# Performance work log

Measured on AMD Instinct MI355X. Metric: run time of the kernel, lower is better.

## Reference

```python
import jax, jax.numpy as jnp
import numpy as np

NUM_PPR_NODES = 262144
BATCH = 4096
K = NUM_PPR_NODES // BATCH  # ppr neighbors per batch node
F_IN, H, C = 256, 512, 64


def setup_inputs() -> dict:
    key = jax.random.key(0)
    ks = jax.random.split(key, 6)
    X = jax.random.normal(ks[0], (NUM_PPR_NODES, F_IN), dtype=jnp.float32)
    ppr_scores = jax.random.uniform(ks[1], (NUM_PPR_NODES,), dtype=jnp.float32)
    # sorted batch ids; last element == BATCH-1 so dim_size = ppr_idx[-1]+1 = BATCH
    ppr_idx = jnp.repeat(jnp.arange(BATCH, dtype=jnp.int64), K)
    s1 = 1.0 / np.sqrt(F_IN)
    s2 = 1.0 / np.sqrt(H)
    Wa = jax.random.uniform(ks[2], (F_IN, H), jnp.float32, -s1, s1)
    Wb = jax.random.uniform(ks[3], (H, H), jnp.float32, -s2, s2)
    Wc = jax.random.uniform(ks[4], (H, H), jnp.float32, -s2, s2)
    Wd = jax.random.uniform(ks[5], (H, C), jnp.float32, -s2, s2)
    return {"X": X, "ppr_scores": ppr_scores, "ppr_idx": ppr_idx,
            "Wa": Wa, "Wb": Wb, "Wc": Wc, "Wd": Wd}


def reference(X, ppr_scores, ppr_idx, Wa, Wb, Wc, Wd):
    # embedding MLP (dropout inactive at eval): Linear -> ReLU -> Linear, no bias
    emb = jax.nn.relu(X @ Wa) @ Wb                      # [N, H]
    # weighted scatter-sum over ppr neighborhoods
    weighted = emb * ppr_scores[:, None]                # [N, H]
    agg = jax.ops.segment_sum(weighted, ppr_idx, num_segments=BATCH)  # [B, H]
    # logit MLP: Linear -> ReLU -> Linear, no bias
    logits = jax.nn.relu(agg @ Wc) @ Wd                 # [B, C]
    return logits
```

## Files before the change

### kernel.cpp

```cpp
#include <hip/hip_runtime.h>

typedef short bs8 __attribute__((ext_vector_type(8)));
typedef float fx4 __attribute__((ext_vector_type(4)));

__device__ __forceinline__ unsigned short f2bf(float f) {
    unsigned u = __builtin_bit_cast(unsigned, f);
    u += 0x7FFFu + ((u >> 16) & 1u);
    return (unsigned short)(u >> 16);
}

__device__ __forceinline__ bs8 load_cvt8_nt(const float* p) {
    fx4 u = __builtin_nontemporal_load((const fx4*)p);
    fx4 v = __builtin_nontemporal_load((const fx4*)(p + 4));
    bs8 r;
    r[0] = (short)f2bf(u[0]); r[1] = (short)f2bf(u[1]);
    r[2] = (short)f2bf(u[2]); r[3] = (short)f2bf(u[3]);
    r[4] = (short)f2bf(v[0]); r[5] = (short)f2bf(v[1]);
    r[6] = (short)f2bf(v[2]); r[7] = (short)f2bf(v[3]);
    return r;
}

__global__ void pack_b(const float* __restrict__ src, unsigned short* __restrict__ dst,
                       int KN, int N) {
    const int l = threadIdx.x;
    const int lr = l & 15, lg = l >> 4;
    const int bid = blockIdx.x;
    const int cf = bid / KN, kc = bid % KN;
    const int col  = cf * 16 + lr;
    const int krow = kc * 32 + lg * 8;
    const size_t ob = ((size_t)bid * 64 + l) * 8;
    #pragma unroll
    for (int j = 0; j < 8; ++j)
        dst[ob + j] = f2bf(src[(size_t)(krow + j) * N + col]);
}

__global__ __launch_bounds__(256) void warm(const float* __restrict__ p, float* __restrict__ sink) {
    float s = p[blockIdx.x * 256 + threadIdx.x];
    if (s == 1e30f) sink[0] = s;
}

__global__ __launch_bounds__(256) void wbc_gemm(const float* __restrict__ Wb,
                                                const float* __restrict__ Wc,
                                                float* __restrict__ Wbc) {
    __shared__ float As[32][33];
    __shared__ float Bs[32][33];
    const int tx = threadIdx.x & 15, ty = threadIdx.x >> 4;
    const int i0 = blockIdx.y * 32, j0 = blockIdx.x * 32;
    float c00 = 0.f, c01 = 0.f, c10 = 0.f, c11 = 0.f;
    for (int k0 = 0; k0 < 512; k0 += 32) {
        for (int t = threadIdx.x; t < 1024; t += 256) {
            int r = t >> 5, c = t & 31;
            As[r][c] = Wb[(size_t)(i0 + r) * 512 + k0 + c];
            Bs[r][c] = Wc[(size_t)(k0 + r) * 512 + j0 + c];
        }
        __syncthreads();
        #pragma unroll
        for (int k = 0; k < 32; ++k) {
            float a0 = As[ty * 2][k], a1 = As[ty * 2 + 1][k];
            float b0 = Bs[k][tx * 2], b1 = Bs[k][tx * 2 + 1];
            c00 += a0 * b0; c01 += a0 * b1; c10 += a1 * b0; c11 += a1 * b1;
        }
        __syncthreads();
    }
    Wbc[(size_t)(i0 + ty * 2) * 512 + j0 + tx * 2]         = c00;
    Wbc[(size_t)(i0 + ty * 2) * 512 + j0 + tx * 2 + 1]     = c01;
    Wbc[(size_t)(i0 + ty * 2 + 1) * 512 + j0 + tx * 2]     = c10;
    Wbc[(size_t)(i0 + ty * 2 + 1) * 512 + j0 + tx * 2 + 1] = c11;
}

__global__ __launch_bounds__(256, 4) void k1_fused(
    const float* __restrict__ X, const float* __restrict__ scores,
    const bs8* __restrict__ WaP, unsigned short* __restrict__ aggH) {
    __shared__ unsigned short xt[16384];

    const int tid = threadIdx.x;
    const int seg = blockIdx.x;
    const size_t row0 = (size_t)seg * 64;

    #pragma unroll
    for (int it = 0; it < 8; ++it) {
        const int flat = it * 2048 + tid * 8;
        const int r = flat >> 8, c = flat & 255;
        bs8 v = load_cvt8_nt(X + (row0 + r) * 256 + c);
        int byte = r * 512 + c * 2;
        byte ^= (r & 7) << 4;
        *(bs8*)((char*)xt + byte) = v;
    }
    __syncthreads();

    const int w = tid >> 6, l = tid & 63;
    const int lr = l & 15, lg = l >> 4;

    #pragma unroll 1
    for (int ci = 0; ci < 4; ++ci) {
        const int c32 = w * 4 + ci;
        fx4 acc0[4], acc1[4];
        #pragma unroll
        for (int mf = 0; mf < 4; ++mf) {
            acc0[mf] = (fx4){0.f, 0.f, 0.f, 0.f};
            acc1[mf] = (fx4){0.f, 0.f, 0.f, 0.f};
        }

        const bs8* bp = WaP + (size_t)c32 * 16 * 64 + l;
        #pragma unroll 1
        for (int kc = 0; kc < 8; ++kc) {
            bs8 b0 = bp[kc * 64];
            bs8 b1 = bp[(8 + kc) * 64];
            bs8 a[4];
            #pragma unroll
            for (int mf = 0; mf < 4; ++mf) {
                const int row = mf * 16 + lr;
                const int x = row * 512 + kc * 64 + lg * 16;
                a[mf] = *(const bs8*)((const char*)xt + (x ^ ((row & 7) << 4)));
            }
            #pragma unroll
            for (int mf = 0; mf < 4; ++mf) {
                acc0[mf] = __builtin_amdgcn_mfma_f32_16x16x32_bf16(a[mf], b0, acc0[mf], 0, 0, 0);
                acc1[mf] = __builtin_amdgcn_mfma_f32_16x16x32_bf16(a[mf], b1, acc1[mf], 0, 0, 0);
            }
        }

        float sc0[4][4];
        #pragma unroll
        for (int mf = 0; mf < 4; ++mf) {
            fx4 sv = *(const fx4*)(scores + row0 + mf * 16 + lg * 4);
            sc0[mf][0] = sv[0]; sc0[mf][1] = sv[1]; sc0[mf][2] = sv[2]; sc0[mf][3] = sv[3];
        }
        float p0 = 0.f, p1 = 0.f;
        #pragma unroll
        for (int mf = 0; mf < 4; ++mf)
            #pragma unroll
            for (int r = 0; r < 4; ++r) {
                float v0 = acc0[mf][r], v1 = acc1[mf][r];
                v0 = v0 > 0.f ? v0 : 0.f;
                v1 = v1 > 0.f ? v1 : 0.f;
                p0 += v0 * sc0[mf][r];
                p1 += v1 * sc0[mf][r];
            }
        p0 += __shfl_xor(p0, 16, 64);
        p0 += __shfl_xor(p0, 32, 64);
        p1 += __shfl_xor(p1, 16, 64);
        p1 += __shfl_xor(p1, 32, 64);
        if (lg == 0) {
            aggH[(size_t)seg * 512 + c32 * 32 + lr]      = f2bf(p0);
            aggH[(size_t)seg * 512 + c32 * 32 + 16 + lr] = f2bf(p1);
        }
    }
}

__global__ __launch_bounds__(256) void k2_gemm(
    const unsigned short* __restrict__ aggH, const bs8* __restrict__ WbcP,
    unsigned short* __restrict__ T) {
    const int tid = threadIdx.x;
    const int w = tid >> 6, l = tid & 63, lr = l & 15, lg = l >> 4;
    const int gw = blockIdx.x * 4 + w;
    const int rg = gw >> 3, cg = gw & 7;
    const int r0 = rg * 64, c0 = cg * 64;

    fx4 acc[4][4];
    #pragma unroll
    for (int mf = 0; mf < 4; ++mf)
        #pragma unroll
        for (int nf = 0; nf < 4; ++nf)
            acc[mf][nf] = (fx4){0.f, 0.f, 0.f, 0.f};

    #pragma unroll 1
    for (int kc = 0; kc < 16; ++kc) {
        bs8 a[4], b[4];
        #pragma unroll
        for (int mf = 0; mf < 4; ++mf)
            a[mf] = *(const bs8*)(aggH + (size_t)(r0 + mf * 16 + lr) * 512 + kc * 32 + lg * 8);
        #pragma unroll
        for (int nf = 0; nf < 4; ++nf)
            b[nf] = WbcP[((cg * 4 + nf) * 16 + kc) * 64 + l];
        #pragma unroll
        for (int mf = 0; mf < 4; ++mf)
            #pragma unroll
            for (int nf = 0; nf < 4; ++nf)
                acc[mf][nf] = __builtin_amdgcn_mfma_f32_16x16x32_bf16(
                    a[mf], b[nf], acc[mf][nf], 0, 0, 0);
    }
    #pragma unroll
    for (int mf = 0; mf < 4; ++mf)
        #pragma unroll
        for (int nf = 0; nf < 4; ++nf)
            #pragma unroll
            for (int r = 0; r < 4; ++r) {
                float v = fmaxf(acc[mf][nf][r], 0.f);
                T[(size_t)(r0 + mf * 16 + lg * 4 + r) * 512 + c0 + nf * 16 + lr] = f2bf(v);
            }
}

__global__ __launch_bounds__(256) void k3_gemm(
    const unsigned short* __restrict__ T, const bs8* __restrict__ WdP,
    float* __restrict__ out) {
    const int tid = threadIdx.x;
    const int w = tid >> 6, l = tid & 63, lr = l & 15, lg = l >> 4;
    const int gw = blockIdx.x * 4 + w;
    const int r0 = gw * 64;

    fx4 acc[4][4];
    #pragma unroll
    for (int mf = 0; mf < 4; ++mf)
        #pragma unroll
        for (int nf = 0; nf < 4; ++nf)
            acc[mf][nf] = (fx4){0.f, 0.f, 0.f, 0.f};

    #pragma unroll 1
    for (int kc = 0; kc < 16; ++kc) {
        bs8 a[4], b[4];
        #pragma unroll
        for (int mf = 0; mf < 4; ++mf)
            a[mf] = *(const bs8*)(T + (size_t)(r0 + mf * 16 + lr) * 512 + kc * 32 + lg * 8);
        #pragma unroll
        for (int nf = 0; nf < 4; ++nf)
            b[nf] = WdP[(nf * 16 + kc) * 64 + l];
        #pragma unroll
        for (int mf = 0; mf < 4; ++mf)
            #pragma unroll
            for (int nf = 0; nf < 4; ++nf)
                acc[mf][nf] = __builtin_amdgcn_mfma_f32_16x16x32_bf16(
                    a[mf], b[nf], acc[mf][nf], 0, 0, 0);
    }
    #pragma unroll
    for (int mf = 0; mf < 4; ++mf)
        #pragma unroll
        for (int nf = 0; nf < 4; ++nf)
            #pragma unroll
            for (int r = 0; r < 4; ++r)
                out[(size_t)(r0 + mf * 16 + lg * 4 + r) * 64 + nf * 16 + lr] = acc[mf][nf][r];
}

extern "C" void kernel_launch(void* const* d_in, const int* in_sizes, int n_in,
                              void* d_out, int out_size, void* d_ws, size_t ws_size,
                              hipStream_t stream) {
    const float* X  = (const float*)d_in[0];
    const float* sc = (const float*)d_in[1];
    const float* Wa = (const float*)d_in[3];
    const float* Wb = (const float*)d_in[4];
    const float* Wc = (const float*)d_in[5];
    const float* Wd = (const float*)d_in[6];
    float* out = (float*)d_out;

    char* ws = (char*)d_ws;
    unsigned short* WaP  = (unsigned short*)(ws + 0);
    unsigned short* WbcP = (unsigned short*)(ws + 262144);
    unsigned short* WdP  = (unsigned short*)(ws + 786432);
    float*          Wbc  = (float*)         (ws + 851968);
    unsigned short* aggH = (unsigned short*)(ws + 1900544);
    unsigned short* T    = (unsigned short*)(ws + 6094848);
    float*          sink = (float*)         (ws + 11534336);

    pack_b<<<dim3(32 * 8),  dim3(64), 0, stream>>>(Wa,  WaP,  8,  512);
    wbc_gemm<<<dim3(16, 16), dim3(256), 0, stream>>>(Wb, Wc, Wbc);
    pack_b<<<dim3(32 * 16), dim3(64), 0, stream>>>(Wbc, WbcP, 16, 512);
    pack_b<<<dim3(4 * 16),  dim3(64), 0, stream>>>(Wd,  WdP,  16, 64);

    warm<<<dim3(256), dim3(256), 0, stream>>>((const float*)WaP, sink);

    k1_fused<<<dim3(4096), dim3(256), 0, stream>>>(X, sc, (const bs8*)WaP, aggH);
    k2_gemm<<<dim3(128),   dim3(256), 0, stream>>>(aggH, (const bs8*)WbcP, T);
    k3_gemm<<<dim3(16),    dim3(256), 0, stream>>>(T, (const bs8*)WdP, out);
}
```

Measured before the change: 176.0 us.

## Replicate packed Wa across eight copies and preload B fragments in k1

The packed Wa weights are replicated into eight copies in the workspace, and each k1 block reads the copy chosen by blockIdx mod 8, so concurrent blocks spread their weight reads over different addresses and cache channels. The k1 inner loop now loads all sixteen B fragments for a column chunk into registers before the MFMA loop and fully unrolls it, so global loads overlap with compute. Launch bounds drop to three blocks per CU to make room for the extra registers, and the warm kernel grows to touch every replica. The costs are more workspace, extra pack work and lower occupancy.

```diff
diff --git a/kernel.cpp b/kernel.cpp
--- a/kernel.cpp
+++ b/kernel.cpp
@@ -21,7 +21,7 @@
 }
 
 __global__ void pack_b(const float* __restrict__ src, unsigned short* __restrict__ dst,
-                       int KN, int N) {
+                       int KN, int N, int nrep, int rep_stride) {
     const int l = threadIdx.x;
     const int lr = l & 15, lg = l >> 4;
     const int bid = blockIdx.x;
@@ -29,9 +29,14 @@
     const int col  = cf * 16 + lr;
     const int krow = kc * 32 + lg * 8;
     const size_t ob = ((size_t)bid * 64 + l) * 8;
+    unsigned short v[8];
     #pragma unroll
     for (int j = 0; j < 8; ++j)
-        dst[ob + j] = f2bf(src[(size_t)(krow + j) * N + col]);
+        v[j] = f2bf(src[(size_t)(krow + j) * N + col]);
+    for (int rep = 0; rep < nrep; ++rep)
+        #pragma unroll
+        for (int j = 0; j < 8; ++j)
+            dst[(size_t)rep * rep_stride + ob + j] = v[j];
 }
 
 __global__ __launch_bounds__(256) void warm(const float* __restrict__ p, float* __restrict__ sink) {
@@ -68,7 +73,7 @@
     Wbc[(size_t)(i0 + ty * 2 + 1) * 512 + j0 + tx * 2 + 1] = c11;
 }
 
-__global__ __launch_bounds__(256, 4) void k1_fused(
+__global__ __launch_bounds__(256, 3) void k1_fused(
     const float* __restrict__ X, const float* __restrict__ scores,
     const bs8* __restrict__ WaP, unsigned short* __restrict__ aggH) {
     __shared__ unsigned short xt[16384];
@@ -76,6 +81,7 @@
     const int tid = threadIdx.x;
     const int seg = blockIdx.x;
     const size_t row0 = (size_t)seg * 64;
+    const bs8* wp = WaP + (size_t)(blockIdx.x & 7) * 16384;
 
     #pragma unroll
     for (int it = 0; it < 8; ++it) {
@@ -94,6 +100,14 @@
     #pragma unroll 1
     for (int ci = 0; ci < 4; ++ci) {
         const int c32 = w * 4 + ci;
+
+        const bs8* bp = wp + (size_t)c32 * 16 * 64 + l;
+        bs8 b0[8], b1[8];
+        #pragma unroll
+        for (int kc = 0; kc < 8; ++kc) b0[kc] = bp[kc * 64];
+        #pragma unroll
+        for (int kc = 0; kc < 8; ++kc) b1[kc] = bp[(8 + kc) * 64];
+
         fx4 acc0[4], acc1[4];
         #pragma unroll
         for (int mf = 0; mf < 4; ++mf) {
@@ -101,11 +115,8 @@
             acc1[mf] = (fx4){0.f, 0.f, 0.f, 0.f};
         }
 
-        const bs8* bp = WaP + (size_t)c32 * 16 * 64 + l;
-        #pragma unroll 1
+        #pragma unroll
         for (int kc = 0; kc < 8; ++kc) {
-            bs8 b0 = bp[kc * 64];
-            bs8 b1 = bp[(8 + kc) * 64];
             bs8 a[4];
             #pragma unroll
             for (int mf = 0; mf < 4; ++mf) {
@@ -115,8 +126,8 @@
             }
             #pragma unroll
             for (int mf = 0; mf < 4; ++mf) {
-                acc0[mf] = __builtin_amdgcn_mfma_f32_16x16x32_bf16(a[mf], b0, acc0[mf], 0, 0, 0);
-                acc1[mf] = __builtin_amdgcn_mfma_f32_16x16x32_bf16(a[mf], b1, acc1[mf], 0, 0, 0);
+                acc0[mf] = __builtin_amdgcn_mfma_f32_16x16x32_bf16(a[mf], b0[kc], acc0[mf], 0, 0, 0);
+                acc1[mf] = __builtin_amdgcn_mfma_f32_16x16x32_bf16(a[mf], b1[kc], acc1[mf], 0, 0, 0);
             }
         }
 
@@ -244,19 +255,19 @@
 
     char* ws = (char*)d_ws;
     unsigned short* WaP  = (unsigned short*)(ws + 0);
-    unsigned short* WbcP = (unsigned short*)(ws + 262144);
-    unsigned short* WdP  = (unsigned short*)(ws + 786432);
-    float*          Wbc  = (float*)         (ws + 851968);
-    unsigned short* aggH = (unsigned short*)(ws + 1900544);
-    unsigned short* T    = (unsigned short*)(ws + 6094848);
-    float*          sink = (float*)         (ws + 11534336);
-
-    pack_b<<<dim3(32 * 8),  dim3(64), 0, stream>>>(Wa,  WaP,  8,  512);
+    unsigned short* WbcP = (unsigned short*)(ws + 2097152);
+    unsigned short* WdP  = (unsigned short*)(ws + 2621440);
+    float*          Wbc  = (float*)         (ws + 2686976);
+    unsigned short* aggH = (unsigned short*)(ws + 3735552);
+    unsigned short* T    = (unsigned short*)(ws + 7929856);
+    float*          sink = (float*)         (ws + 12124160);
+
+    pack_b<<<dim3(32 * 8),  dim3(64), 0, stream>>>(Wa,  WaP,  8,  512, 8, 131072);
     wbc_gemm<<<dim3(16, 16), dim3(256), 0, stream>>>(Wb, Wc, Wbc);
-    pack_b<<<dim3(32 * 16), dim3(64), 0, stream>>>(Wbc, WbcP, 16, 512);
-    pack_b<<<dim3(4 * 16),  dim3(64), 0, stream>>>(Wd,  WdP,  16, 64);
-
-    warm<<<dim3(256), dim3(256), 0, stream>>>((const float*)WaP, sink);
+    pack_b<<<dim3(32 * 16), dim3(64), 0, stream>>>(Wbc, WbcP, 16, 512, 1, 0);
+    pack_b<<<dim3(4 * 16),  dim3(64), 0, stream>>>(Wd,  WdP,  16, 64, 1, 0);
+
+    warm<<<dim3(2048), dim3(256), 0, stream>>>((const float*)WaP, sink);
 
     k1_fused<<<dim3(4096), dim3(256), 0, stream>>>(X, sc, (const bs8*)WaP, aggH);
     k2_gemm<<<dim3(128),   dim3(256), 0, stream>>>(aggH, (const bs8*)WbcP, T);
```

Measured after the change: 346.3 us. 1.97x slower.
